# Kernel tuning notes

Hardware: AMD Instinct MI355X
Metric: run time of the kernel (lower is better)

## Reference

```python
import jax, jax.numpy as jnp
import numpy as np

D_K = 64
N_HEADS = 16
D_MODEL = 1024
EPS = 1e-5


def setup_inputs() -> dict:
    key = jax.random.key(0)
    ks = jax.random.split(key, 8)
    B, S = 2, 2048
    scale = 1.0 / np.sqrt(D_MODEL)
    inp = {
        "input_Q": jax.random.normal(ks[0], (B, S, D_MODEL), jnp.float32),
        "input_K": jax.random.normal(ks[1], (B, S, D_MODEL), jnp.float32),
        "input_V": jax.random.normal(ks[2], (B, S, D_MODEL), jnp.float32),
        "attn_mask": jax.random.randint(ks[3], (B, S, S), 0, 2) == 1,
        "W_Q": jax.random.normal(ks[4], (D_MODEL, N_HEADS * D_K), jnp.float32) * scale,
        "W_K": jax.random.normal(ks[5], (D_MODEL, N_HEADS * D_K), jnp.float32) * scale,
        "W_V": jax.random.normal(ks[6], (D_MODEL, N_HEADS * D_K), jnp.float32) * scale,
        "W_fc": jax.random.normal(ks[7], (N_HEADS * D_K, D_MODEL), jnp.float32) * scale,
    }
    return inp


def _layer_norm(x):
    mu = jnp.mean(x, axis=-1, keepdims=True)
    var = jnp.var(x, axis=-1, keepdims=True)
    return (x - mu) / jnp.sqrt(var + EPS)


def reference(input_Q, input_K, input_V, attn_mask, W_Q, W_K, W_V, W_fc):
    B, S, _ = input_Q.shape
    # projections -> [B, H, S, d_k]
    Q = (input_Q @ W_Q).reshape(B, S, N_HEADS, D_K).transpose(0, 2, 1, 3)
    K = (input_K @ W_K).reshape(B, S, N_HEADS, D_K).transpose(0, 2, 1, 3)
    V = (input_V @ W_V).reshape(B, S, N_HEADS, D_K).transpose(0, 2, 1, 3)
    scores = jnp.einsum("bhqd,bhkd->bhqk", Q, K) / np.sqrt(D_K)
    scores = jnp.where(attn_mask[:, None, :, :], -1e9, scores)
    attn = jax.nn.softmax(scores, axis=-1)
    context = jnp.einsum("bhqk,bhkd->bhqd", attn, V)
    context = context.transpose(0, 2, 1, 3).reshape(B, S, N_HEADS * D_K)
    output = context @ W_fc
    return _layer_norm(output + input_Q), attn
```

## Files before the change

### kernel.cpp

```cpp
#include <hip/hip_runtime.h>

typedef __bf16 bf16x8 __attribute__((ext_vector_type(8)));
typedef unsigned short u16x8 __attribute__((ext_vector_type(8)));
typedef float f32x4 __attribute__((ext_vector_type(4)));

#define DEV static __device__ __forceinline__

DEV unsigned short f2bf(float f) {
  union { float f; unsigned u; } v; v.f = f;
  unsigned u = v.u + 0x7FFFu + ((v.u >> 16) & 1u);
  return (unsigned short)(u >> 16);
}

DEV int swz(int row, int k) { return row * 64 + (k ^ ((row & 7) * 8)); }

#define GLOAD16(gp, lp)                                                        \
  __builtin_amdgcn_global_load_lds(                                            \
      (const __attribute__((address_space(1))) void*)(const void*)(gp),        \
      (__attribute__((address_space(3))) void*)(void*)(lp), 16, 0, 0)

__global__ __launch_bounds__(256) void k_detect(const unsigned* m, int* flag) {
  __shared__ int sF, sI;
  if (threadIdx.x == 0) { sF = 1; sI = 1; }
  __syncthreads();
  int lF = 1, lI = 1;
  for (int i = threadIdx.x; i < 4096; i += 256) {
    unsigned d = m[i];
    lF &= (d == 0u || d == 0x3F800000u);
    lI &= (d == 0u || d == 1u);
  }
  if (!lF) atomicAnd(&sF, 0);
  if (!lI) atomicAnd(&sI, 0);
  __syncthreads();
  if (threadIdx.x == 0) flag[0] = sF ? 2 : (sI ? 0 : 1);
}

__global__ __launch_bounds__(256) void k_pack(const void* m, const int* flag,
                                              unsigned long long* bits) {
  const int tid = threadIdx.x;
  const int w = blockIdx.x * 4 + (tid >> 6);
  const int lane = tid & 63;
  const size_t idx = (size_t)w * 64 + lane;
  const int fl = flag[0];
  int v;
  if (fl == 1)      v = ((const unsigned char*)m)[idx];
  else if (fl == 0) v = ((const int*)m)[idx];
  else              v = (((const float*)m)[idx] != 0.f);
  unsigned long long bal = __ballot(v != 0);
  if (lane == 0) bits[w] = bal;
}

__global__ __launch_bounds__(256) void k_cvt(const float* a, const float* b,
                                             const float* c, unsigned short* out) {
  const int gid = blockIdx.x * 256 + threadIdx.x;
  const int which = gid >> 20;
  const int loc = gid & 1048575;
  const float* src = which == 0 ? a : which == 1 ? b : c;
  float4 f = ((const float4*)src)[loc];
  ushort4 u = make_ushort4(f2bf(f.x), f2bf(f.y), f2bf(f.z), f2bf(f.w));
  *(ushort4*)(out + (size_t)which * 4194304 + (size_t)loc * 4) = u;
}

__global__ __launch_bounds__(256) void k_wt(const float* w0, const float* w1,
                                            const float* w2, const float* w3,
                                            unsigned short* out) {
  __shared__ float t[32][33];
  const int z = blockIdx.z;
  const float* W = z == 0 ? w0 : z == 1 ? w1 : z == 2 ? w2 : w3;
  unsigned short* Wt = out + (size_t)z * 1048576;
  const int x = threadIdx.x, y = threadIdx.y;
  const int k0 = blockIdx.x * 32, n0 = blockIdx.y * 32;
#pragma unroll
  for (int r = 0; r < 4; ++r)
    t[y + r * 8][x] = W[(size_t)(k0 + y + r * 8) * 1024 + n0 + x];
  __syncthreads();
#pragma unroll
  for (int r = 0; r < 4; ++r)
    Wt[(size_t)(n0 + y + r * 8) * 1024 + k0 + x] = f2bf(t[x][y + r * 8]);
}

__global__ __launch_bounds__(256) void k_gemm(
    const unsigned short* __restrict__ A0, const unsigned short* __restrict__ A1,
    const unsigned short* __restrict__ A2, const unsigned short* __restrict__ B0,
    const unsigned short* __restrict__ B1, const unsigned short* __restrict__ B2,
    unsigned short* __restrict__ C0, unsigned short* __restrict__ C1,
    unsigned short* __restrict__ C2, float* __restrict__ Cf) {
  __shared__ __align__(16) unsigned short As[128 * 64];
  __shared__ __align__(16) unsigned short Bs[128 * 64];
  const int z = blockIdx.z;
  const unsigned short* A = z == 0 ? A0 : z == 1 ? A1 : A2;
  const unsigned short* Bt = z == 0 ? B0 : z == 1 ? B1 : B2;
  unsigned short* Cb = z == 0 ? C0 : z == 1 ? C1 : C2;

  const int tid = threadIdx.x, lane = tid & 63, wid = tid >> 6;
  const int mt = blockIdx.x, nt = blockIdx.y;
  const int wm = (wid >> 1) * 64, wn = (wid & 1) * 64;
  const int lr = lane >> 3;
  const int lc = ((lane & 7) ^ (lane >> 3)) * 8;
  const int l15 = lane & 15, lg = lane >> 4;
  f32x4 acc[4][4] = {};

  for (int kt = 0; kt < 16; ++kt) {
    const int k0 = kt * 64;
#pragma unroll
    for (int c = wid; c < 16; c += 4) {
      GLOAD16(A + (size_t)(mt * 128 + c * 8 + lr) * 1024 + k0 + lc, As + c * 512);
      GLOAD16(Bt + (size_t)(nt * 128 + c * 8 + lr) * 1024 + k0 + lc, Bs + c * 512);
    }
    __syncthreads();
#pragma unroll
    for (int ks = 0; ks < 2; ++ks) {
      const int ko = ks * 32 + lg * 8;
      bf16x8 af[4], bfr[4];
#pragma unroll
      for (int f = 0; f < 4; ++f) {
        af[f] = *(const bf16x8*)(As + swz(wm + f * 16 + l15, ko));
        bfr[f] = *(const bf16x8*)(Bs + swz(wn + f * 16 + l15, ko));
      }
#pragma unroll
      for (int i = 0; i < 4; ++i)
#pragma unroll
        for (int j = 0; j < 4; ++j)
          acc[i][j] = __builtin_amdgcn_mfma_f32_16x16x32_bf16(af[i], bfr[j],
                                                              acc[i][j], 0, 0, 0);
    }
    __syncthreads();
  }
  const int rbase = mt * 128 + wm + lg * 4;
  const int cbase = nt * 128 + wn + l15;
#pragma unroll
  for (int i = 0; i < 4; ++i)
#pragma unroll
    for (int j = 0; j < 4; ++j) {
      const int col = cbase + j * 16;
#pragma unroll
      for (int r = 0; r < 4; ++r) {
        const int row = rbase + i * 16 + r;
        if (Cf) Cf[(size_t)row * 1024 + col] = acc[i][j][r];
        else    Cb[(size_t)row * 1024 + col] = f2bf(acc[i][j][r]);
      }
    }
}

__global__ __launch_bounds__(256) void k_attn(
    const unsigned short* __restrict__ PQ, const unsigned short* __restrict__ PK,
    const unsigned short* __restrict__ PV_, const unsigned long long* __restrict__ bits,
    float* __restrict__ attn_out, unsigned short* __restrict__ CTX) {
  __shared__ __align__(16) unsigned short Qs[64 * 64];
  __shared__ __align__(16) unsigned short Ks[64 * 64];
  __shared__ __align__(16) unsigned short Vts[64 * 64];
  __shared__ __align__(16) unsigned short Ps[4][16 * 64];

  const int tid = threadIdx.x, lane = tid & 63, wid = tid >> 6;
  const int qt = blockIdx.x, h = blockIdx.y, b = blockIdx.z;
  const int q0 = qt * 64;
  const int lr = lane >> 3;
  const int lc = ((lane & 7) ^ (lane >> 3)) * 8;
  const int l15 = lane & 15, lg = lane >> 4;

#pragma unroll
  for (int c = wid; c < 8; c += 4)
    GLOAD16(PQ + (size_t)(b * 2048 + q0 + c * 8 + lr) * 1024 + h * 64 + lc, Qs + c * 512);
  __syncthreads();
  const bf16x8 qf0 = *(const bf16x8*)(Qs + swz(wid * 16 + l15, lg * 8));
  const bf16x8 qf1 = *(const bf16x8*)(Qs + swz(wid * 16 + l15, 32 + lg * 8));
  const unsigned long long* mrow =
      bits + (size_t)(b * 2048 + q0 + wid * 16 + lg * 4) * 32;

  float rs[4] = {0.f, 0.f, 0.f, 0.f};
  for (int kt = 0; kt < 32; ++kt) {
    __syncthreads();
#pragma unroll
    for (int c = wid; c < 8; c += 4)
      GLOAD16(PK + (size_t)(b * 2048 + kt * 64 + c * 8 + lr) * 1024 + h * 64 + lc,
              Ks + c * 512);
    __syncthreads();
    const unsigned long long w0 = mrow[kt], w1 = mrow[32 + kt],
                             w2 = mrow[64 + kt], w3 = mrow[96 + kt];
#pragma unroll
    for (int fn = 0; fn < 4; ++fn) {
      const bf16x8 kf0 = *(const bf16x8*)(Ks + swz(fn * 16 + l15, lg * 8));
      const bf16x8 kf1 = *(const bf16x8*)(Ks + swz(fn * 16 + l15, 32 + lg * 8));
      f32x4 s = {};
      s = __builtin_amdgcn_mfma_f32_16x16x32_bf16(qf0, kf0, s, 0, 0, 0);
      s = __builtin_amdgcn_mfma_f32_16x16x32_bf16(qf1, kf1, s, 0, 0, 0);
      const int kb = fn * 16 + l15;
      rs[0] += ((w0 >> kb) & 1) ? 0.f : __expf(s[0] * 0.125f);
      rs[1] += ((w1 >> kb) & 1) ? 0.f : __expf(s[1] * 0.125f);
      rs[2] += ((w2 >> kb) & 1) ? 0.f : __expf(s[2] * 0.125f);
      rs[3] += ((w3 >> kb) & 1) ? 0.f : __expf(s[3] * 0.125f);
    }
  }
#pragma unroll
  for (int r = 0; r < 4; ++r) {
#pragma unroll
    for (int m = 1; m < 16; m <<= 1) rs[r] += __shfl_xor(rs[r], m);
    rs[r] = 1.f / rs[r];
  }

  f32x4 cacc[4] = {};
  for (int kt = 0; kt < 32; ++kt) {
    const int k0 = kt * 64;
    __syncthreads();
#pragma unroll
    for (int c = wid; c < 8; c += 4)
      GLOAD16(PK + (size_t)(b * 2048 + k0 + c * 8 + lr) * 1024 + h * 64 + lc,
              Ks + c * 512);
#pragma unroll
    for (int i = 0; i < 2; ++i) {
      const int vr = i * 32 + (tid >> 3);
      const int d0 = (tid & 7) * 8;
      u16x8 vv = *(const u16x8*)(PV_ + (size_t)(b * 2048 + k0 + vr) * 1024 + h * 64 + d0);
#pragma unroll
      for (int e = 0; e < 8; ++e) Vts[swz(d0 + e, vr)] = vv[e];
    }
    __syncthreads();
    const unsigned long long wm_[4] = {mrow[kt], mrow[32 + kt], mrow[64 + kt],
                                       mrow[96 + kt]};
#pragma unroll
    for (int fn = 0; fn < 4; ++fn) {
      const bf16x8 kf0 = *(const bf16x8*)(Ks + swz(fn * 16 + l15, lg * 8));
      const bf16x8 kf1 = *(const bf16x8*)(Ks + swz(fn * 16 + l15, 32 + lg * 8));
      f32x4 s = {};
      s = __builtin_amdgcn_mfma_f32_16x16x32_bf16(qf0, kf0, s, 0, 0, 0);
      s = __builtin_amdgcn_mfma_f32_16x16x32_bf16(qf1, kf1, s, 0, 0, 0);
      const int kb = fn * 16 + l15;
#pragma unroll
      for (int r = 0; r < 4; ++r) {
        const float p =
            ((wm_[r] >> kb) & 1) ? 0.f : __expf(s[r] * 0.125f) * rs[r];
        const int q = q0 + wid * 16 + lg * 4 + r;
        attn_out[((size_t)(b * 16 + h) * 2048 + q) * 2048 + k0 + kb] = p;
        Ps[wid][swz(lg * 4 + r, kb)] = f2bf(p);
      }
    }
#pragma unroll
    for (int ks = 0; ks < 2; ++ks) {
      const int ko = ks * 32 + lg * 8;
      const bf16x8 pf = *(const bf16x8*)(&Ps[wid][swz(l15, ko)]);
#pragma unroll
      for (int fn = 0; fn < 4; ++fn) {
        const bf16x8 vf = *(const bf16x8*)(Vts + swz(fn * 16 + l15, ko));
        cacc[fn] = __builtin_amdgcn_mfma_f32_16x16x32_bf16(pf, vf, cacc[fn], 0, 0, 0);
      }
    }
  }
#pragma unroll
  for (int fn = 0; fn < 4; ++fn)
#pragma unroll
    for (int r = 0; r < 4; ++r) {
      const int q = q0 + wid * 16 + lg * 4 + r;
      CTX[(size_t)(b * 2048 + q) * 1024 + h * 64 + fn * 16 + l15] =
          f2bf(cacc[fn][r]);
    }
}

__global__ __launch_bounds__(256) void k_ln(const float* __restrict__ PRE,
                                            const float* __restrict__ inQ,
                                            float* __restrict__ out) {
  const int row = blockIdx.x, tid = threadIdx.x;
  const size_t base = (size_t)row * 1024 + tid * 4;
  const float4 x = *(const float4*)(PRE + base);
  const float4 q = *(const float4*)(inQ + base);
  const float v0 = x.x + q.x, v1 = x.y + q.y, v2 = x.z + q.z, v3 = x.w + q.w;
  float s = v0 + v1 + v2 + v3;
  float ss = v0 * v0 + v1 * v1 + v2 * v2 + v3 * v3;
#pragma unroll
  for (int m = 1; m < 64; m <<= 1) {
    s += __shfl_xor(s, m);
    ss += __shfl_xor(ss, m);
  }
  __shared__ float red[8];
  const int wid = tid >> 6, lane = tid & 63;
  if (lane == 0) { red[wid] = s; red[4 + wid] = ss; }
  __syncthreads();
  if (tid == 0) {
    const float S = red[0] + red[1] + red[2] + red[3];
    const float SS = red[4] + red[5] + red[6] + red[7];
    const float mu = S * (1.f / 1024.f);
    const float var = SS * (1.f / 1024.f) - mu * mu;
    red[0] = mu;
    red[1] = rsqrtf(var + 1e-5f);
  }
  __syncthreads();
  const float mu = red[0], rstd = red[1];
  float4 o;
  o.x = (v0 - mu) * rstd; o.y = (v1 - mu) * rstd;
  o.z = (v2 - mu) * rstd; o.w = (v3 - mu) * rstd;
  *(float4*)(out + base) = o;
}

extern "C" void kernel_launch(void* const* d_in, const int* in_sizes, int n_in,
                              void* d_out, int out_size, void* d_ws, size_t ws_size,
                              hipStream_t stream) {
  const float* inQ = (const float*)d_in[0];
  const float* inK = (const float*)d_in[1];
  const float* inV = (const float*)d_in[2];
  const void* msk = d_in[3];
  const float* wq = (const float*)d_in[4];
  const float* wk = (const float*)d_in[5];
  const float* wv = (const float*)d_in[6];
  const float* wf = (const float*)d_in[7];

  char* ws = (char*)d_ws;
  unsigned short* XQ = (unsigned short*)(ws);
  unsigned short* WT = (unsigned short*)(ws + 25165824);
  unsigned short* PQ = (unsigned short*)(ws + 33554432);
  unsigned short* PK = (unsigned short*)(ws + 41943040);
  unsigned short* PV = (unsigned short*)(ws + 50331648);
  unsigned short* CTX = (unsigned short*)(ws + 58720256);
  float* PRE = (float*)(ws + 67108864);
  unsigned long long* BITS = (unsigned long long*)(ws + 83886080);
  int* FLAG = (int*)(ws + 84934656);

  float* outLN = (float*)d_out;
  float* outAT = (float*)d_out + 4194304;

  k_detect<<<1, 256, 0, stream>>>((const unsigned*)msk, FLAG);
  k_pack<<<32768, 256, 0, stream>>>(msk, FLAG, BITS);
  k_cvt<<<12288, 256, 0, stream>>>(inQ, inK, inV, XQ);
  k_wt<<<dim3(32, 32, 4), dim3(32, 8, 1), 0, stream>>>(wq, wk, wv, wf, WT);
  k_gemm<<<dim3(32, 8, 3), 256, 0, stream>>>(XQ, XQ + 4194304, XQ + 8388608,
                                             WT, WT + 1048576, WT + 2097152,
                                             PQ, PK, PV, nullptr);
  k_attn<<<dim3(32, 16, 2), 256, 0, stream>>>(PQ, PK, PV, BITS, outAT, CTX);
  k_gemm<<<dim3(32, 8, 1), 256, 0, stream>>>(CTX, CTX, CTX, WT + 3145728,
                                             WT + 3145728, WT + 3145728,
                                             nullptr, nullptr, nullptr, PRE);
  k_ln<<<4096, 256, 0, stream>>>(PRE, inQ, outLN);
}
```

Baseline: 415.4 us.

## Double-buffer K/V tiles in attention and vectorize attn probability stores

The attention kernel now double-buffers K and V tiles in shared memory, prefetching the next tile while the current one is computed, which cuts one barrier per iteration. The exp is replaced by a hardware exp2 with a folded scale constant. The attention-probability output is written as coalesced float4 stores read back from the bf16 P tile instead of scattered scalar stores. This changes the stored attn values to bf16-rounded precision, which is a possible accuracy risk, and it uses more LDS.

```diff
diff --git a/kernel.cpp b/kernel.cpp
--- a/kernel.cpp
+++ b/kernel.cpp
@@ -2,6 +2,7 @@
 
 typedef __bf16 bf16x8 __attribute__((ext_vector_type(8)));
 typedef unsigned short u16x8 __attribute__((ext_vector_type(8)));
+typedef unsigned short u16x4 __attribute__((ext_vector_type(4)));
 typedef float f32x4 __attribute__((ext_vector_type(4)));
 
 #define DEV static __device__ __forceinline__
@@ -11,6 +12,13 @@
   unsigned u = v.u + 0x7FFFu + ((v.u >> 16) & 1u);
   return (unsigned short)(u >> 16);
 }
+
+DEV float bf2f(unsigned short b) {
+  union { unsigned u; float f; } v; v.u = ((unsigned)b) << 16;
+  return v.f;
+}
+
+DEV float fast_exp2(float x) { return __builtin_amdgcn_exp2f(x); }
 
 DEV int swz(int row, int k) { return row * 64 + (k ^ ((row & 7) * 8)); }
 
@@ -146,9 +154,8 @@
     const unsigned short* __restrict__ PQ, const unsigned short* __restrict__ PK,
     const unsigned short* __restrict__ PV_, const unsigned long long* __restrict__ bits,
     float* __restrict__ attn_out, unsigned short* __restrict__ CTX) {
-  __shared__ __align__(16) unsigned short Qs[64 * 64];
-  __shared__ __align__(16) unsigned short Ks[64 * 64];
-  __shared__ __align__(16) unsigned short Vts[64 * 64];
+  __shared__ __align__(16) unsigned short KB[2][64 * 64];
+  __shared__ __align__(16) unsigned short VB[2][64 * 64];
   __shared__ __align__(16) unsigned short Ps[4][16 * 64];
 
   const int tid = threadIdx.x, lane = tid & 63, wid = tid >> 6;
@@ -157,39 +164,50 @@
   const int lr = lane >> 3;
   const int lc = ((lane & 7) ^ (lane >> 3)) * 8;
   const int l15 = lane & 15, lg = lane >> 4;
+  const size_t rowK = (size_t)(b * 2048) * 1024 + h * 64;
+  const float C = 0.125f * 1.44269504f;
 
 #pragma unroll
   for (int c = wid; c < 8; c += 4)
-    GLOAD16(PQ + (size_t)(b * 2048 + q0 + c * 8 + lr) * 1024 + h * 64 + lc, Qs + c * 512);
-  __syncthreads();
-  const bf16x8 qf0 = *(const bf16x8*)(Qs + swz(wid * 16 + l15, lg * 8));
-  const bf16x8 qf1 = *(const bf16x8*)(Qs + swz(wid * 16 + l15, 32 + lg * 8));
+    GLOAD16(PQ + rowK + (size_t)(q0 + c * 8 + lr) * 1024 + lc, KB[0] + c * 512);
+  __syncthreads();
+  const bf16x8 qf0 = *(const bf16x8*)(KB[0] + swz(wid * 16 + l15, lg * 8));
+  const bf16x8 qf1 = *(const bf16x8*)(KB[0] + swz(wid * 16 + l15, 32 + lg * 8));
   const unsigned long long* mrow =
       bits + (size_t)(b * 2048 + q0 + wid * 16 + lg * 4) * 32;
+  __syncthreads();
+
+#pragma unroll
+  for (int c = wid; c < 8; c += 4)
+    GLOAD16(PK + rowK + (size_t)(c * 8 + lr) * 1024 + lc, KB[0] + c * 512);
+  __syncthreads();
 
   float rs[4] = {0.f, 0.f, 0.f, 0.f};
+  int cur = 0;
   for (int kt = 0; kt < 32; ++kt) {
-    __syncthreads();
-#pragma unroll
-    for (int c = wid; c < 8; c += 4)
-      GLOAD16(PK + (size_t)(b * 2048 + kt * 64 + c * 8 + lr) * 1024 + h * 64 + lc,
-              Ks + c * 512);
-    __syncthreads();
+    if (kt < 31) {
+#pragma unroll
+      for (int c = wid; c < 8; c += 4)
+        GLOAD16(PK + rowK + (size_t)((kt + 1) * 64 + c * 8 + lr) * 1024 + lc,
+                KB[cur ^ 1] + c * 512);
+    }
     const unsigned long long w0 = mrow[kt], w1 = mrow[32 + kt],
                              w2 = mrow[64 + kt], w3 = mrow[96 + kt];
 #pragma unroll
     for (int fn = 0; fn < 4; ++fn) {
-      const bf16x8 kf0 = *(const bf16x8*)(Ks + swz(fn * 16 + l15, lg * 8));
-      const bf16x8 kf1 = *(const bf16x8*)(Ks + swz(fn * 16 + l15, 32 + lg * 8));
+      const bf16x8 kf0 = *(const bf16x8*)(KB[cur] + swz(fn * 16 + l15, lg * 8));
+      const bf16x8 kf1 = *(const bf16x8*)(KB[cur] + swz(fn * 16 + l15, 32 + lg * 8));
       f32x4 s = {};
       s = __builtin_amdgcn_mfma_f32_16x16x32_bf16(qf0, kf0, s, 0, 0, 0);
       s = __builtin_amdgcn_mfma_f32_16x16x32_bf16(qf1, kf1, s, 0, 0, 0);
       const int kb = fn * 16 + l15;
-      rs[0] += ((w0 >> kb) & 1) ? 0.f : __expf(s[0] * 0.125f);
-      rs[1] += ((w1 >> kb) & 1) ? 0.f : __expf(s[1] * 0.125f);
-      rs[2] += ((w2 >> kb) & 1) ? 0.f : __expf(s[2] * 0.125f);
-      rs[3] += ((w3 >> kb) & 1) ? 0.f : __expf(s[3] * 0.125f);
-    }
+      rs[0] += ((w0 >> kb) & 1) ? 0.f : fast_exp2(s[0] * C);
+      rs[1] += ((w1 >> kb) & 1) ? 0.f : fast_exp2(s[1] * C);
+      rs[2] += ((w2 >> kb) & 1) ? 0.f : fast_exp2(s[2] * C);
+      rs[3] += ((w3 >> kb) & 1) ? 0.f : fast_exp2(s[3] * C);
+    }
+    __syncthreads();
+    cur ^= 1;
   }
 #pragma unroll
   for (int r = 0; r < 4; ++r) {
@@ -198,29 +216,41 @@
     rs[r] = 1.f / rs[r];
   }
 
+  const int vr = tid >> 3, d0 = (tid & 7) * 8;
+  {
+#pragma unroll
+    for (int c = wid; c < 8; c += 4)
+      GLOAD16(PK + rowK + (size_t)(c * 8 + lr) * 1024 + lc, KB[0] + c * 512);
+    u16x8 v0 = *(const u16x8*)(PV_ + rowK + (size_t)vr * 1024 + d0);
+    u16x8 v1 = *(const u16x8*)(PV_ + rowK + (size_t)(32 + vr) * 1024 + d0);
+#pragma unroll
+    for (int e = 0; e < 8; ++e) VB[0][swz(d0 + e, vr)] = v0[e];
+#pragma unroll
+    for (int e = 0; e < 8; ++e) VB[0][swz(d0 + e, 32 + vr)] = v1[e];
+    __syncthreads();
+  }
+
   f32x4 cacc[4] = {};
+  cur = 0;
+  const int srow = lane >> 2, scg = lane & 3;
+  float* arow = attn_out + ((size_t)(b * 16 + h) * 2048 + q0 + wid * 16 + srow) * 2048;
   for (int kt = 0; kt < 32; ++kt) {
     const int k0 = kt * 64;
-    __syncthreads();
-#pragma unroll
-    for (int c = wid; c < 8; c += 4)
-      GLOAD16(PK + (size_t)(b * 2048 + k0 + c * 8 + lr) * 1024 + h * 64 + lc,
-              Ks + c * 512);
-#pragma unroll
-    for (int i = 0; i < 2; ++i) {
-      const int vr = i * 32 + (tid >> 3);
-      const int d0 = (tid & 7) * 8;
-      u16x8 vv = *(const u16x8*)(PV_ + (size_t)(b * 2048 + k0 + vr) * 1024 + h * 64 + d0);
-#pragma unroll
-      for (int e = 0; e < 8; ++e) Vts[swz(d0 + e, vr)] = vv[e];
-    }
-    __syncthreads();
+    u16x8 nv0, nv1;
+    if (kt < 31) {
+      const size_t nb = rowK + (size_t)((kt + 1) * 64) * 1024;
+      nv0 = *(const u16x8*)(PV_ + nb + (size_t)vr * 1024 + d0);
+      nv1 = *(const u16x8*)(PV_ + nb + (size_t)(32 + vr) * 1024 + d0);
+#pragma unroll
+      for (int c = wid; c < 8; c += 4)
+        GLOAD16(PK + nb + (size_t)(c * 8 + lr) * 1024 + lc, KB[cur ^ 1] + c * 512);
+    }
     const unsigned long long wm_[4] = {mrow[kt], mrow[32 + kt], mrow[64 + kt],
                                        mrow[96 + kt]};
 #pragma unroll
     for (int fn = 0; fn < 4; ++fn) {
-      const bf16x8 kf0 = *(const bf16x8*)(Ks + swz(fn * 16 + l15, lg * 8));
-      const bf16x8 kf1 = *(const bf16x8*)(Ks + swz(fn * 16 + l15, 32 + lg * 8));
+      const bf16x8 kf0 = *(const bf16x8*)(KB[cur] + swz(fn * 16 + l15, lg * 8));
+      const bf16x8 kf1 = *(const bf16x8*)(KB[cur] + swz(fn * 16 + l15, 32 + lg * 8));
       f32x4 s = {};
       s = __builtin_amdgcn_mfma_f32_16x16x32_bf16(qf0, kf0, s, 0, 0, 0);
       s = __builtin_amdgcn_mfma_f32_16x16x32_bf16(qf1, kf1, s, 0, 0, 0);
@@ -228,11 +258,17 @@
 #pragma unroll
       for (int r = 0; r < 4; ++r) {
         const float p =
-            ((wm_[r] >> kb) & 1) ? 0.f : __expf(s[r] * 0.125f) * rs[r];
-        const int q = q0 + wid * 16 + lg * 4 + r;
-        attn_out[((size_t)(b * 16 + h) * 2048 + q) * 2048 + k0 + kb] = p;
+            ((wm_[r] >> kb) & 1) ? 0.f : fast_exp2(s[r] * C) * rs[r];
         Ps[wid][swz(lg * 4 + r, kb)] = f2bf(p);
       }
+    }
+#pragma unroll
+    for (int j = 0; j < 4; ++j) {
+      const int c = scg * 4 + j * 16;
+      const u16x4 pb = *(const u16x4*)(&Ps[wid][swz(srow, c)]);
+      float4 o;
+      o.x = bf2f(pb[0]); o.y = bf2f(pb[1]); o.z = bf2f(pb[2]); o.w = bf2f(pb[3]);
+      *(float4*)(arow + k0 + c) = o;
     }
 #pragma unroll
     for (int ks = 0; ks < 2; ++ks) {
@@ -240,10 +276,18 @@
       const bf16x8 pf = *(const bf16x8*)(&Ps[wid][swz(l15, ko)]);
 #pragma unroll
       for (int fn = 0; fn < 4; ++fn) {
-        const bf16x8 vf = *(const bf16x8*)(Vts + swz(fn * 16 + l15, ko));
+        const bf16x8 vf = *(const bf16x8*)(VB[cur] + swz(fn * 16 + l15, ko));
         cacc[fn] = __builtin_amdgcn_mfma_f32_16x16x32_bf16(pf, vf, cacc[fn], 0, 0, 0);
       }
     }
+    if (kt < 31) {
+#pragma unroll
+      for (int e = 0; e < 8; ++e) VB[cur ^ 1][swz(d0 + e, vr)] = nv0[e];
+#pragma unroll
+      for (int e = 0; e < 8; ++e) VB[cur ^ 1][swz(d0 + e, 32 + vr)] = nv1[e];
+    }
+    __syncthreads();
+    cur ^= 1;
   }
 #pragma unroll
   for (int fn = 0; fn < 4; ++fn)
```

Measured after the change: 396.9 us. -4.4%, faster.
